# Kernel tuning notes

Hardware: AMD Instinct MI355X
Metric: run time of the kernel (lower is better)

## Reference

```python
import jax, jax.numpy as jnp
import numpy as np

N_NODES = 50000
D = 128
N_EDGES = 800000


def _gcn_layer(h, W, b, row, col, mask, n_nodes):
    # Linear: h @ W.T + b  (nn.Linear convention)
    h = h @ W.T + b
    # degree of source nodes, counting only non-self-loop edges (remove_self_loops)
    deg = jax.ops.segment_sum(mask.astype(h.dtype), row, num_segments=n_nodes)
    deg_inv_sqrt = jnp.where(deg > 0, jax.lax.rsqrt(jnp.maximum(deg, 1.0)), 0.0)
    norm = deg_inv_sqrt[row] * deg_inv_sqrt[col] * mask.astype(h.dtype)
    # gather-scale messages [E, D], scatter-add into target nodes (col)
    msg = norm[:, None] * h[row]
    return jax.ops.segment_sum(msg, col, num_segments=n_nodes)


def setup_inputs() -> dict:
    key = jax.random.key(0)
    ks = jax.random.split(key, 9)
    x = jax.random.normal(ks[0], (N_NODES, D), dtype=jnp.float32)
    edge_index = jax.random.randint(ks[1], (2, N_EDGES), 0, N_NODES, dtype=jnp.int64)
    lim = 1.0 / np.sqrt(D)
    params = {}
    for i in range(3):
        params[f"W{i}"] = jax.random.uniform(ks[2 + 2 * i], (D, D), jnp.float32, -lim, lim)
        params[f"b{i}"] = jax.random.uniform(ks[3 + 2 * i], (D,), jnp.float32, -lim, lim)
    return {"x": x, "edge_index": edge_index, **params}


def reference(x, edge_index, W0, b0, W1, b1, W2, b2):
    row, col = edge_index[0], edge_index[1]
    mask = row != col  # remove_self_loops
    h = x
    for W, b in ((W0, b0), (W1, b1), (W2, b2)):
        h_new = jax.nn.relu(_gcn_layer(h, W, b, row, col, mask, x.shape[0]))
        h = h + h_new
    return h
```

## Files before the change

### kernel.cpp

```cpp
#include <hip/hip_runtime.h>
#include <hip/hip_bf16.h>


#define D_DIM 128
#define SCAN_CHUNK 1024
#define CHUNKS 256
#define GROUPS 8
#define GS (CHUNKS / GROUPS)
#define LDSW 12512

typedef __attribute__((ext_vector_type(8))) short bf16x8;
typedef __attribute__((ext_vector_type(4))) float f32x4;

static __device__ __forceinline__ short f2bf(float f) {
    union { __hip_bfloat16 b; short s; } u;
    u.b = __float2bfloat16(f);
    return u.s;
}
static __device__ __forceinline__ float bf_lo(unsigned p) { return __uint_as_float(p << 16); }
static __device__ __forceinline__ float bf_hi(unsigned p) { return __uint_as_float(p & 0xffff0000u); }


__global__ __launch_bounds__(256) void hist_kernel(const int* __restrict__ ei,
                                                   unsigned* __restrict__ partial_col,
                                                   unsigned* __restrict__ partial_row,
                                                   const float* __restrict__ W0,
                                                   const float* __restrict__ W1,
                                                   const float* __restrict__ W2,
                                                   unsigned short* __restrict__ Wb,
                                                   const float* __restrict__ x,
                                                   const float* __restrict__ b0,
                                                   unsigned short* __restrict__ hWb,
                                                   int nrows, int E, int CHSZ) {
    __shared__ unsigned hh[LDSW];
    int tid = threadIdx.x;
    if (blockIdx.y == 2) {
        int i = blockIdx.x * 256 + tid;
        if (i < 3 * D_DIM * D_DIM) {
            const float* W = (i < 16384) ? W0 : (i < 32768) ? W1 : W2;
            Wb[i] = (unsigned short)f2bf(W[i & 16383]);
        }
        return;
    }
    if (blockIdx.y == 3) {
        int wave = tid >> 6;
        int lane = tid & 63;
        int r0 = blockIdx.x * 64 + wave * 16;
        if (r0 >= nrows) return;
        int m = lane & 15, q = lane >> 4;
        int rload = min(r0 + m, nrows - 1);
        const float4* h4 = (const float4*)x;
        const float4* w4 = (const float4*)W0;

        f32x4 acc[8];
#pragma unroll
        for (int jt = 0; jt < 8; jt++) acc[jt] = (f32x4){0.f, 0.f, 0.f, 0.f};

#pragma unroll
        for (int k0 = 0; k0 < 128; k0 += 32) {
            int c0 = k0 + q * 8;
            float4 x0 = h4[rload * 32 + (c0 >> 2)];
            float4 x1 = h4[rload * 32 + (c0 >> 2) + 1];
            bf16x8 a;
            a[0] = f2bf(x0.x); a[1] = f2bf(x0.y); a[2] = f2bf(x0.z); a[3] = f2bf(x0.w);
            a[4] = f2bf(x1.x); a[5] = f2bf(x1.y); a[6] = f2bf(x1.z); a[7] = f2bf(x1.w);
#pragma unroll
            for (int jt = 0; jt < 8; jt++) {
                float4 w0v = w4[(jt * 16 + m) * 32 + (c0 >> 2)];
                float4 w1v = w4[(jt * 16 + m) * 32 + (c0 >> 2) + 1];
                bf16x8 b;
                b[0] = f2bf(w0v.x); b[1] = f2bf(w0v.y); b[2] = f2bf(w0v.z); b[3] = f2bf(w0v.w);
                b[4] = f2bf(w1v.x); b[5] = f2bf(w1v.y); b[6] = f2bf(w1v.z); b[7] = f2bf(w1v.w);
                acc[jt] = __builtin_amdgcn_mfma_f32_16x16x32_bf16(a, b, acc[jt], 0, 0, 0);
            }
        }
        unsigned short* stg = (unsigned short*)hh + wave * 16 * 136;
#pragma unroll
        for (int jt = 0; jt < 8; jt++) {
            float bv = b0[jt * 16 + m];
#pragma unroll
            for (int reg = 0; reg < 4; reg++)
                stg[(q * 4 + reg) * 136 + jt * 16 + m] =
                    (unsigned short)f2bf(acc[jt][reg] + bv);
        }
#pragma unroll
        for (int t = 0; t < 4; t++) {
            int rl = t * 4 + (lane >> 4);
            int gr = r0 + rl;
            if (gr < nrows) {
                uint4 v = *(const uint4*)&stg[rl * 136 + (lane & 15) * 8];
                *(uint4*)&hWb[(size_t)gr * D_DIM + (lane & 15) * 8] = v;
            }
        }
        return;
    }
    int ch = blockIdx.x;
    if (ch >= CHUNKS) return;
    int docol = (blockIdx.y == 0);
    for (int i = tid; i < LDSW; i += 256) hh[i] = 0u;
    __syncthreads();
    int e0 = ch * CHSZ, e1 = min(e0 + CHSZ, E);
    for (int e = e0 + tid; e < e1; e += 256) {
        int row = ei[e];
        int col = ei[E + e];
        if (row == col) continue;
        int bin = docol ? col : row;
        atomicAdd(&hh[bin >> 2], 1u << ((bin & 3) * 8));
    }
    __syncthreads();
    unsigned* dst = (docol ? partial_col : partial_row) + (size_t)ch * LDSW;
    for (int i = tid; i < LDSW; i += 256) dst[i] = hh[i];
}

__global__ __launch_bounds__(256) void group_prefix_kernel(
    unsigned* __restrict__ partial_col, const unsigned* __restrict__ partial_row,
    unsigned* __restrict__ gsum_col, unsigned* __restrict__ gsum_row, int NW) {
    int w = blockIdx.x * 256 + threadIdx.x;
    if (w >= NW) return;
    int g = blockIdx.y;
    size_t base = (size_t)(g * GS) * LDSW + w;
    if (blockIdx.z == 0) {
        unsigned run = 0;
#pragma unroll 4
        for (int c = 0; c < GS; c++) {
            unsigned v = partial_col[base + (size_t)c * LDSW];
            partial_col[base + (size_t)c * LDSW] = run;
            run += v;
        }
        gsum_col[g * NW + w] = run;
    } else {
        unsigned run = 0;
#pragma unroll 4
        for (int c = 0; c < GS; c++) run += partial_row[base + (size_t)c * LDSW];
        gsum_row[g * NW + w] = run;
    }
}

__global__ __launch_bounds__(256) void cnt_dis_kernel(
    unsigned* __restrict__ gsum_col, const unsigned* __restrict__ gsum_row,
    int* __restrict__ col_cnt, float* __restrict__ dis, int* __restrict__ bsum, int NW) {
    __shared__ int wsum[4];
    int w = blockIdx.x * 256 + threadIdx.x;
    int s = 0;
    if (w < NW) {
        unsigned wcv[GROUPS];
        unsigned clo = 0, chi = 0, rlo = 0, rhi = 0;
#pragma unroll
        for (int g = 0; g < GROUPS; g++) {
            unsigned wc = gsum_col[g * NW + w];
            unsigned wr = gsum_row[g * NW + w];
            wcv[g] = wc;
            clo += wc & 0x00FF00FFu; chi += (wc >> 8) & 0x00FF00FFu;
            rlo += wr & 0x00FF00FFu; rhi += (wr >> 8) & 0x00FF00FFu;
        }
        unsigned run = 0;
#pragma unroll
        for (int g = 0; g < GROUPS; g++) {
            gsum_col[g * NW + w] = run;
            run += wcv[g];
        }
        int c0 = clo & 0xFFFF, c1 = chi & 0xFFFF, c2 = clo >> 16, c3 = chi >> 16;
        int r0 = rlo & 0xFFFF, r1 = rhi & 0xFFFF, r2 = rlo >> 16, r3 = rhi >> 16;
        ((int4*)col_cnt)[w] = make_int4(c0, c1, c2, c3);
        float4 dv;
        dv.x = (r0 > 0) ? rsqrtf((float)r0) : 0.0f;
        dv.y = (r1 > 0) ? rsqrtf((float)r1) : 0.0f;
        dv.z = (r2 > 0) ? rsqrtf((float)r2) : 0.0f;
        dv.w = (r3 > 0) ? rsqrtf((float)r3) : 0.0f;
        ((float4*)dis)[w] = dv;
        s = c0 + c1 + c2 + c3;
    }
#pragma unroll
    for (int d = 32; d > 0; d >>= 1) s += __shfl_down(s, d, 64);
    int lane = threadIdx.x & 63, wv = threadIdx.x >> 6;
    if (lane == 0) wsum[wv] = s;
    __syncthreads();
    if (threadIdx.x == 0) bsum[blockIdx.x] = wsum[0] + wsum[1] + wsum[2] + wsum[3];
}

__global__ __launch_bounds__(256) void scan_final_kernel(const int* __restrict__ cnt,
                                                         const int* __restrict__ bsum,
                                                         int* __restrict__ offs,
                                                         int n, int G) {
    __shared__ int wsum[4];
    __shared__ int sblock;
    int base = blockIdx.x * SCAN_CHUNK;
    int tid = threadIdx.x;
    const int PT = SCAN_CHUNK / 256;
    int v[PT];
    int s = 0;
#pragma unroll
    for (int i = 0; i < PT; i++) {
        int g = base + tid * PT + i;
        v[i] = (g < n) ? cnt[g] : 0;
        s += v[i];
    }
    int local_sum = s;
    int lane = tid & 63, w = tid >> 6;
#pragma unroll
    for (int d = 1; d < 64; d <<= 1) {
        int t = __shfl_up(s, d, 64);
        if (lane >= d) s += t;
    }
    if (lane == 63) wsum[w] = s;
    if (tid < 64) {
        int bv = (tid < G) ? bsum[tid] : 0;
        int bs = bv;
#pragma unroll
        for (int d = 1; d < 64; d <<= 1) {
            int t = __shfl_up(bs, d, 64);
            if (tid >= d) bs += t;
        }
        if (tid == blockIdx.x) sblock = bs - bv;
        if (tid == 63 && blockIdx.x == G - 1) offs[n] = bs;
    }
    __syncthreads();
    int wbase = 0;
    for (int i = 0; i < w; i++) wbase += wsum[i];
    int run = sblock + wbase + (s - local_sum);
#pragma unroll
    for (int i = 0; i < PT; i++) {
        int g = base + tid * PT + i;
        if (g < n) offs[g] = run;
        run += v[i];
    }
}

__global__ __launch_bounds__(256) void scatter_kernel(const int* __restrict__ ei,
                                                      const float* __restrict__ dis,
                                                      const int* __restrict__ offs,
                                                      const unsigned* __restrict__ chpref,
                                                      const unsigned* __restrict__ gpref,
                                                      unsigned* __restrict__ epack,
                                                      int E, int CHSZ, int NW) {
    __shared__ unsigned cur[LDSW];
    int tid = threadIdx.x;
    int ch = blockIdx.x;
    const unsigned* pf = chpref + (size_t)ch * LDSW;
    const unsigned* gb = gpref + (size_t)(ch / GS) * NW;
    for (int i = tid; i < LDSW; i += 256) {
        unsigned seed = pf[i];
        if (i < NW) seed += gb[i];
        cur[i] = seed;
    }
    __syncthreads();
    int e0 = ch * CHSZ, e1 = min(e0 + CHSZ, E);
    for (int e = e0 + tid; e < e1; e += 256) {
        int row = ei[e];
        int col = ei[E + e];
        if (row == col) continue;
        float wgt = dis[row] * dis[col];
        int wd = col >> 2, sh = (col & 3) * 8;
        unsigned old = atomicAdd(&cur[wd], 1u << sh);
        int slot = offs[col] + (int)((old >> sh) & 0xFFu);
        epack[slot] = (unsigned)row | ((unsigned)(unsigned short)f2bf(wgt) << 16);
    }
}


__global__ __launch_bounds__(256) void linear_mfma_kernel(
    const float* __restrict__ A, const unsigned short* __restrict__ Wb,
    const float* __restrict__ bias, unsigned short* __restrict__ hWb, int nrows) {
    __shared__ unsigned short stage[4][16 * 136];
    int wave = threadIdx.x >> 6;
    int lane = threadIdx.x & 63;
    int r0 = blockIdx.x * 64 + wave * 16;
    int m = lane & 15, q = lane >> 4;
    int rload = min(r0 + m, nrows - 1);
    const float4* h4 = (const float4*)A;

    f32x4 acc[8];
#pragma unroll
    for (int jt = 0; jt < 8; jt++) acc[jt] = (f32x4){0.f, 0.f, 0.f, 0.f};

#pragma unroll
    for (int k0 = 0; k0 < 128; k0 += 32) {
        int c0 = k0 + q * 8;
        float4 x0 = h4[rload * 32 + (c0 >> 2)];
        float4 x1 = h4[rload * 32 + (c0 >> 2) + 1];
        bf16x8 a;
        a[0] = f2bf(x0.x); a[1] = f2bf(x0.y); a[2] = f2bf(x0.z); a[3] = f2bf(x0.w);
        a[4] = f2bf(x1.x); a[5] = f2bf(x1.y); a[6] = f2bf(x1.z); a[7] = f2bf(x1.w);
#pragma unroll
        for (int jt = 0; jt < 8; jt++) {
            bf16x8 b = *(const bf16x8*)(Wb + (jt * 16 + m) * D_DIM + c0);
            acc[jt] = __builtin_amdgcn_mfma_f32_16x16x32_bf16(a, b, acc[jt], 0, 0, 0);
        }
    }

#pragma unroll
    for (int jt = 0; jt < 8; jt++) {
        float bv = bias[jt * 16 + m];
#pragma unroll
        for (int reg = 0; reg < 4; reg++)
            stage[wave][(q * 4 + reg) * 136 + jt * 16 + m] =
                (unsigned short)f2bf(acc[jt][reg] + bv);
    }
#pragma unroll
    for (int t = 0; t < 4; t++) {
        int rl = t * 4 + (lane >> 4);
        int gr = r0 + rl;
        if (gr < nrows) {
            uint4 v = *(const uint4*)&stage[wave][rl * 136 + (lane & 15) * 8];
            *(uint4*)&hWb[(size_t)gr * D_DIM + (lane & 15) * 8] = v;
        }
    }
}

__global__ __launch_bounds__(256) void agg_kernel(const int* __restrict__ offs,
                                                  const unsigned* __restrict__ epack,
                                                  const uint4* __restrict__ hW4,
                                                  const float* __restrict__ hprev,
                                                  float* __restrict__ hout, int n_nodes) {
    int node = (int)((blockIdx.x * blockDim.x + threadIdx.x) >> 6);
    int lane = threadIdx.x & 63;
    if (node >= n_nodes) return;
    int g = lane >> 4, s = lane & 15;

    int beg = offs[node];
    int end = offs[node + 1];

    float acc[8];
#pragma unroll
    for (int k = 0; k < 8; k++) acc[k] = 0.f;

    for (int i = beg; i < end; i += 16) {
        int last = end - 1;
        int i0 = i + g, i1 = i0 + 4, i2 = i0 + 8, i3 = i0 + 12;
        unsigned e0 = epack[min(i0, last)];
        unsigned e1 = epack[min(i1, last)];
        unsigned e2 = epack[min(i2, last)];
        unsigned e3 = epack[min(i3, last)];
        uint4 p0 = hW4[(e0 & 0xffffu) * 16 + s];
        uint4 p1 = hW4[(e1 & 0xffffu) * 16 + s];
        uint4 p2 = hW4[(e2 & 0xffffu) * 16 + s];
        uint4 p3 = hW4[(e3 & 0xffffu) * 16 + s];
        float w0 = (i0 < end) ? bf_hi(e0) : 0.f;
        float w1 = (i1 < end) ? bf_hi(e1) : 0.f;
        float w2 = (i2 < end) ? bf_hi(e2) : 0.f;
        float w3 = (i3 < end) ? bf_hi(e3) : 0.f;
        acc[0] = fmaf(w0, bf_lo(p0.x), acc[0]); acc[1] = fmaf(w0, bf_hi(p0.x), acc[1]);
        acc[2] = fmaf(w0, bf_lo(p0.y), acc[2]); acc[3] = fmaf(w0, bf_hi(p0.y), acc[3]);
        acc[4] = fmaf(w0, bf_lo(p0.z), acc[4]); acc[5] = fmaf(w0, bf_hi(p0.z), acc[5]);
        acc[6] = fmaf(w0, bf_lo(p0.w), acc[6]); acc[7] = fmaf(w0, bf_hi(p0.w), acc[7]);
        acc[0] = fmaf(w1, bf_lo(p1.x), acc[0]); acc[1] = fmaf(w1, bf_hi(p1.x), acc[1]);
        acc[2] = fmaf(w1, bf_lo(p1.y), acc[2]); acc[3] = fmaf(w1, bf_hi(p1.y), acc[3]);
        acc[4] = fmaf(w1, bf_lo(p1.z), acc[4]); acc[5] = fmaf(w1, bf_hi(p1.z), acc[5]);
        acc[6] = fmaf(w1, bf_lo(p1.w), acc[6]); acc[7] = fmaf(w1, bf_hi(p1.w), acc[7]);
        acc[0] = fmaf(w2, bf_lo(p2.x), acc[0]); acc[1] = fmaf(w2, bf_hi(p2.x), acc[1]);
        acc[2] = fmaf(w2, bf_lo(p2.y), acc[2]); acc[3] = fmaf(w2, bf_hi(p2.y), acc[3]);
        acc[4] = fmaf(w2, bf_lo(p2.z), acc[4]); acc[5] = fmaf(w2, bf_hi(p2.z), acc[5]);
        acc[6] = fmaf(w2, bf_lo(p2.w), acc[6]); acc[7] = fmaf(w2, bf_hi(p2.w), acc[7]);
        acc[0] = fmaf(w3, bf_lo(p3.x), acc[0]); acc[1] = fmaf(w3, bf_hi(p3.x), acc[1]);
        acc[2] = fmaf(w3, bf_lo(p3.y), acc[2]); acc[3] = fmaf(w3, bf_hi(p3.y), acc[3]);
        acc[4] = fmaf(w3, bf_lo(p3.z), acc[4]); acc[5] = fmaf(w3, bf_hi(p3.z), acc[5]);
        acc[6] = fmaf(w3, bf_lo(p3.w), acc[6]); acc[7] = fmaf(w3, bf_hi(p3.w), acc[7]);
    }

#pragma unroll
    for (int k = 0; k < 8; k++) {
        acc[k] += __shfl_xor(acc[k], 16, 64);
        acc[k] += __shfl_xor(acc[k], 32, 64);
    }

    if (g == 0) {
        const float4* hp4 = (const float4*)hprev;
        float4* ho4 = (float4*)hout;
        int idx = node * 32 + s * 2;
        float4 h0 = hp4[idx], h1 = hp4[idx + 1];
        float4 o0, o1;
        o0.x = h0.x + fmaxf(acc[0], 0.f); o0.y = h0.y + fmaxf(acc[1], 0.f);
        o0.z = h0.z + fmaxf(acc[2], 0.f); o0.w = h0.w + fmaxf(acc[3], 0.f);
        o1.x = h1.x + fmaxf(acc[4], 0.f); o1.y = h1.y + fmaxf(acc[5], 0.f);
        o1.z = h1.z + fmaxf(acc[6], 0.f); o1.w = h1.w + fmaxf(acc[7], 0.f);
        ho4[idx] = o0;
        ho4[idx + 1] = o1;
    }
}


static inline size_t align_up(size_t x, size_t a) { return (x + a - 1) & ~(a - 1); }

extern "C" void kernel_launch(void* const* d_in, const int* in_sizes, int n_in,
                              void* d_out, int out_size, void* d_ws, size_t ws_size,
                              hipStream_t stream) {
    const float* x = (const float*)d_in[0];
    const int* ei = (const int*)d_in[1];
    const float* Wl[3] = {(const float*)d_in[2], (const float*)d_in[4], (const float*)d_in[6]};
    const float* bl[3] = {(const float*)d_in[3], (const float*)d_in[5], (const float*)d_in[7]};

    const int N = in_sizes[0] / D_DIM;
    const int E = in_sizes[1] / 2;
    const int NW = N / 4;
    const int G = (N + SCAN_CHUNK - 1) / SCAN_CHUNK;
    const int NWB = (NW + 255) / 256;
    const int CHSZ = (E + CHUNKS - 1) / CHUNKS;

    char* p = (char*)d_ws;
    int* col_cnt = (int*)p;            p += align_up((size_t)N * 4, 256);
    int* offs    = (int*)p;            p += align_up((size_t)(N + 1) * 4, 256);
    float* dis   = (float*)p;          p += align_up((size_t)N * 4, 256);
    int* bsum    = (int*)p;            p += align_up((size_t)64 * 4, 256);
    unsigned* partial_col = (unsigned*)p;  p += align_up((size_t)CHUNKS * LDSW * 4, 256);
    unsigned* partial_row = (unsigned*)p;  p += align_up((size_t)CHUNKS * LDSW * 4, 256);
    unsigned* gsum_col = (unsigned*)p; p += align_up((size_t)GROUPS * NW * 4, 256);
    unsigned* gsum_row = (unsigned*)p; p += align_up((size_t)GROUPS * NW * 4, 256);
    unsigned short* Wb = (unsigned short*)p;  p += align_up((size_t)3 * D_DIM * D_DIM * 2, 256);
    unsigned* epack = (unsigned*)p;    p += align_up((size_t)E * 4, 256);
    unsigned short* hWb = (unsigned short*)p;  p += align_up((size_t)N * D_DIM * 2, 256);
    (void)ws_size;

    int gemm_blocks = (N + 63) / 64;
    int hist_gx = (gemm_blocks > CHUNKS) ? gemm_blocks : CHUNKS;

    hist_kernel<<<dim3(hist_gx, 4), 256, 0, stream>>>(ei, partial_col, partial_row,
                                                      Wl[0], Wl[1], Wl[2], Wb,
                                                      x, bl[0], hWb, N, E, CHSZ);
    group_prefix_kernel<<<dim3(NWB, GROUPS, 2), 256, 0, stream>>>(partial_col, partial_row,
                                                                  gsum_col, gsum_row, NW);
    cnt_dis_kernel<<<NWB, 256, 0, stream>>>(gsum_col, gsum_row, col_cnt, dis, bsum, NW);
    scan_final_kernel<<<G, 256, 0, stream>>>(col_cnt, bsum, offs, N, G);
    scatter_kernel<<<CHUNKS, 256, 0, stream>>>(ei, dis, offs, partial_col, gsum_col,
                                               epack, E, CHSZ, NW);

    const float* hprev = x;
    float* h = (float*)d_out;
    int agg_blocks = (N + 3) / 4;
    for (int l = 0; l < 3; l++) {
        if (l > 0)
            linear_mfma_kernel<<<gemm_blocks, 256, 0, stream>>>(hprev, Wb + l * 16384,
                                                                bl[l], hWb, N);
        agg_kernel<<<agg_blocks, 256, 0, stream>>>(offs, epack, (const uint4*)hWb, hprev, h, N);
        hprev = h;
    }
}
```

Baseline: 308.2 us.

## Split histogram and scatter LDS bins across blocks to cut LDS footprint

Halves the number of edge chunks and splits each chunk's LDS histogram into two bin halves, and the scatter's counters into four bin quarters, each handled by a separate block that filters edges to its own range. This shrinks per-block LDS so more blocks can be resident and shortens the zero-init and writeback work per block. In exchange every block reads the full chunk of edges, so edge-index reads from global memory double in the histogram pass and quadruple in the scatter pass. The halved chunk count also doubles the per-chunk counts held in the 8-bit packed bins, which raises the risk of overflow.

```diff
diff --git a/kernel.cpp b/kernel.cpp
--- a/kernel.cpp
+++ b/kernel.cpp
@@ -4,10 +4,16 @@
 
 #define D_DIM 128
 #define SCAN_CHUNK 1024
-#define CHUNKS 256
+#define CHUNKS 128
 #define GROUPS 8
 #define GS (CHUNKS / GROUPS)
 #define LDSW 12512
+#define HALVES 2
+#define HWRD (LDSW / HALVES)
+#define HBINS (HWRD * 4)
+#define QUARTERS 4
+#define QWRD (LDSW / QUARTERS)
+#define QBINS (QWRD * 4)
 
 typedef __attribute__((ext_vector_type(8))) short bf16x8;
 typedef __attribute__((ext_vector_type(4))) float f32x4;
@@ -32,9 +38,9 @@
                                                    const float* __restrict__ b0,
                                                    unsigned short* __restrict__ hWb,
                                                    int nrows, int E, int CHSZ) {
-    __shared__ unsigned hh[LDSW];
+    __shared__ unsigned hh[HWRD];
     int tid = threadIdx.x;
-    if (blockIdx.y == 2) {
+    if (blockIdx.y == 4) {
         int i = blockIdx.x * 256 + tid;
         if (i < 3 * D_DIM * D_DIM) {
             const float* W = (i < 16384) ? W0 : (i < 32768) ? W1 : W2;
@@ -42,7 +48,7 @@
         }
         return;
     }
-    if (blockIdx.y == 3) {
+    if (blockIdx.y == 5) {
         int wave = tid >> 6;
         int lane = tid & 63;
         int r0 = blockIdx.x * 64 + wave * 16;
@@ -96,20 +102,23 @@
     }
     int ch = blockIdx.x;
     if (ch >= CHUNKS) return;
-    int docol = (blockIdx.y == 0);
-    for (int i = tid; i < LDSW; i += 256) hh[i] = 0u;
+    int docol = (blockIdx.y < 2);
+    int half = blockIdx.y & 1;
+    int bin0 = half * HBINS;
+    for (int i = tid; i < HWRD; i += 256) hh[i] = 0u;
     __syncthreads();
     int e0 = ch * CHSZ, e1 = min(e0 + CHSZ, E);
     for (int e = e0 + tid; e < e1; e += 256) {
         int row = ei[e];
         int col = ei[E + e];
         if (row == col) continue;
-        int bin = docol ? col : row;
-        atomicAdd(&hh[bin >> 2], 1u << ((bin & 3) * 8));
+        int rb = (docol ? col : row) - bin0;
+        if ((unsigned)rb < (unsigned)HBINS)
+            atomicAdd(&hh[rb >> 2], 1u << ((rb & 3) * 8));
     }
     __syncthreads();
-    unsigned* dst = (docol ? partial_col : partial_row) + (size_t)ch * LDSW;
-    for (int i = tid; i < LDSW; i += 256) dst[i] = hh[i];
+    unsigned* dst = (docol ? partial_col : partial_row) + (size_t)ch * LDSW + half * HWRD;
+    for (int i = tid; i < HWRD; i += 256) dst[i] = hh[i];
 }
 
 __global__ __launch_bounds__(256) void group_prefix_kernel(
@@ -233,14 +242,18 @@
                                                       const unsigned* __restrict__ gpref,
                                                       unsigned* __restrict__ epack,
                                                       int E, int CHSZ, int NW) {
-    __shared__ unsigned cur[LDSW];
+    __shared__ unsigned cur[QWRD];
     int tid = threadIdx.x;
     int ch = blockIdx.x;
-    const unsigned* pf = chpref + (size_t)ch * LDSW;
+    int q = blockIdx.y;
+    int wbase = q * QWRD;
+    int bin0 = q * QBINS;
+    const unsigned* pf = chpref + (size_t)ch * LDSW + wbase;
     const unsigned* gb = gpref + (size_t)(ch / GS) * NW;
-    for (int i = tid; i < LDSW; i += 256) {
+    for (int i = tid; i < QWRD; i += 256) {
         unsigned seed = pf[i];
-        if (i < NW) seed += gb[i];
+        int w = wbase + i;
+        if (w < NW) seed += gb[w];
         cur[i] = seed;
     }
     __syncthreads();
@@ -249,8 +262,10 @@
         int row = ei[e];
         int col = ei[E + e];
         if (row == col) continue;
+        int rb = col - bin0;
+        if ((unsigned)rb >= (unsigned)QBINS) continue;
         float wgt = dis[row] * dis[col];
-        int wd = col >> 2, sh = (col & 3) * 8;
+        int wd = rb >> 2, sh = (rb & 3) * 8;
         unsigned old = atomicAdd(&cur[wd], 1u << sh);
         int slot = offs[col] + (int)((old >> sh) & 0xFFu);
         epack[slot] = (unsigned)row | ((unsigned)(unsigned short)f2bf(wgt) << 16);
@@ -411,17 +426,17 @@
     (void)ws_size;
 
     int gemm_blocks = (N + 63) / 64;
-    int hist_gx = (gemm_blocks > CHUNKS) ? gemm_blocks : CHUNKS;
-
-    hist_kernel<<<dim3(hist_gx, 4), 256, 0, stream>>>(ei, partial_col, partial_row,
+    int hist_gx = gemm_blocks;
+
+    hist_kernel<<<dim3(hist_gx, 6), 256, 0, stream>>>(ei, partial_col, partial_row,
                                                       Wl[0], Wl[1], Wl[2], Wb,
                                                       x, bl[0], hWb, N, E, CHSZ);
     group_prefix_kernel<<<dim3(NWB, GROUPS, 2), 256, 0, stream>>>(partial_col, partial_row,
                                                                   gsum_col, gsum_row, NW);
     cnt_dis_kernel<<<NWB, 256, 0, stream>>>(gsum_col, gsum_row, col_cnt, dis, bsum, NW);
     scan_final_kernel<<<G, 256, 0, stream>>>(col_cnt, bsum, offs, N, G);
-    scatter_kernel<<<CHUNKS, 256, 0, stream>>>(ei, dis, offs, partial_col, gsum_col,
-                                               epack, E, CHSZ, NW);
+    scatter_kernel<<<dim3(CHUNKS, QUARTERS), 256, 0, stream>>>(ei, dis, offs, partial_col,
+                                                               gsum_col, epack, E, CHSZ, NW);
 
     const float* hprev = x;
     float* h = (float*)d_out;
```

After: 294.2 us. -4.6%, faster.
